# Performance work log

Hardware: AMD Instinct MI355X
Metric: run time of the kernel (lower is better)

The kernel has to match this reference:

```python
import jax, jax.numpy as jnp
import numpy as np
import math

B, C, H, W = 2, 512, 64, 64
NUM_HEADS = 8
D_K = C // NUM_HEADS
SCALE = 1.0 / math.sqrt(D_K)


def setup_inputs() -> dict:
    key = jax.random.key(0)
    ks = jax.random.split(key, 7)
    init = 0.02
    return {
        "x": jax.random.normal(ks[0], (B, C, H, W), dtype=jnp.float32),
        "Wq": jax.random.normal(ks[1], (C, C), dtype=jnp.float32) * init,
        "bq": jnp.zeros((C,), dtype=jnp.float32),
        "Wkv": jax.random.normal(ks[2], (2 * C, C), dtype=jnp.float32) * init,
        "bkv": jnp.zeros((2 * C,), dtype=jnp.float32),
        "Wp": jax.random.normal(ks[3], (C, C), dtype=jnp.float32) * init,
        "bp": jnp.zeros((C,), dtype=jnp.float32),
    }


def _conv1x1(x, w, b):
    # x: [b, c_in, h, w], w: [c_out, c_in] (1x1 conv kernel), b: [c_out]
    return jnp.einsum('bchw,oc->bohw', x, w) + b[None, :, None, None]


def reference(x, Wq, bq, Wkv, bkv, Wp, bp):
    b, c, h, w = x.shape
    l = h * w
    q = _conv1x1(x, Wq, bq)
    kv = _conv1x1(x, Wkv, bkv)
    k, v = jnp.split(kv, 2, axis=1)
    # reshape to [b, heads, d_k, l]
    q = q.reshape(b, NUM_HEADS, D_K, l)
    k = k.reshape(b, NUM_HEADS, D_K, l)
    v = v.reshape(b, NUM_HEADS, D_K, l)
    attn = jnp.einsum('bhct,bhcs->bhts', q, k) * SCALE  # [b,h,l,l]
    attn = jax.nn.softmax(attn, axis=-1)
    out = jnp.einsum('bhts,bhcs->bhct', attn, v)  # [b,h,d_k,l]
    out = out.reshape(b, c, h, w)
    out = _conv1x1(out, Wp, bp)
    return out
```

## Files before the change

kernel.cpp:

```cpp
#include <hip/hip_runtime.h>
#include <math.h>

#define L_SEQ 4096
#define C_DIM 512
#define NH 8
#define DK 64
#define NB 2
#define QSC 0.18033688011112042f

typedef _Float16 f16;
typedef _Float16 f16x8 __attribute__((ext_vector_type(8)));
typedef _Float16 f16x4 __attribute__((ext_vector_type(4)));
typedef __fp16 h16x2 __attribute__((ext_vector_type(2)));
typedef float f32x4 __attribute__((ext_vector_type(4)));
typedef float f32x16 __attribute__((ext_vector_type(16)));
typedef unsigned int u32;

__global__ __launch_bounds__(256) void prep(
    const float* __restrict__ X, const float* __restrict__ Wq,
    const float* __restrict__ Wkv, const float* __restrict__ Wp,
    f16* __restrict__ Xt, f16* __restrict__ Wqkh,
    f16* __restrict__ Wvh, f16* __restrict__ Wph)
{
    const int tid = threadIdx.x;
    const int z = blockIdx.z;
    if (z < 2) {
        __shared__ f16 Ts[64][72];
        const float* src = X + (size_t)z * C_DIM * L_SEQ;
        f16* dst = Xt + (size_t)z * L_SEQ * C_DIM;
        for (int tile = blockIdx.x; tile < 512; tile += gridDim.x) {
            const int c0 = (tile & 7) * 64;
            const int t0 = (tile >> 3) * 64;
            __syncthreads();
            #pragma unroll
            for (int p = 0; p < 4; ++p) {
                const int c = (tid >> 4) + p * 16;
                const int t = (tid & 15) * 4;
                const float4 v = *(const float4*)(src + (size_t)(c0 + c) * L_SEQ + t0 + t);
                Ts[t + 0][c] = (f16)v.x; Ts[t + 1][c] = (f16)v.y;
                Ts[t + 2][c] = (f16)v.z; Ts[t + 3][c] = (f16)v.w;
            }
            __syncthreads();
            #pragma unroll
            for (int p = 0; p < 2; ++p) {
                const int t = (tid >> 3) + p * 32;
                const int ch = (tid & 7) * 8;
                *(f16x8*)(dst + (size_t)(t0 + t) * C_DIM + c0 + ch) =
                    *(const f16x8*)&Ts[t][ch];
            }
        }
    } else {
        const float* srcs[4] = {Wq, Wkv, Wkv + 262144, Wp};
        f16* dsts[4] = {Wqkh, Wqkh + 262144, Wvh, Wph};
        #pragma unroll
        for (int s = 0; s < 4; ++s) {
            const float* sp = srcs[s]; f16* dp = dsts[s];
            for (int i = blockIdx.x * 256 + tid; i < 65536; i += gridDim.x * 256) {
                const float4 v = *(const float4*)(sp + (size_t)i * 4);
                f16x4 h; h[0] = (f16)v.x; h[1] = (f16)v.y; h[2] = (f16)v.z; h[3] = (f16)v.w;
                *(f16x4*)(dp + (size_t)i * 4) = h;
            }
        }
    }
}

__global__ __launch_bounds__(256) void qkv_mfma(
    const f16* __restrict__ Xt, const f16* __restrict__ Wqkv,
    const float* __restrict__ bq, const float* __restrict__ bkv,
    f16* __restrict__ Qh, f16* __restrict__ Kh, f16* __restrict__ Vh)
{
    __shared__ f16 As[128][40];
    __shared__ f16 Bs[128][40];
    const int tid = threadIdx.x;
    const int lane = tid & 63, w = tid >> 6;
    const int l15 = lane & 15, quad = lane >> 4;
    const int wy = w >> 1, wx = w & 1;
    const int mb0 = blockIdx.x * 128;
    const int n0  = blockIdx.y * 128;

    f32x4 acc[4][4] = {};
    const int row = tid >> 2, c8 = (tid & 3) * 8;
    const f16* aptr = Xt + (size_t)mb0 * 512;
    const f16* bptr = Wqkv + (size_t)n0 * 512;

    uint4 ga0 = *(const uint4*)(aptr + (size_t)row * 512 + c8);
    uint4 ga1 = *(const uint4*)(aptr + (size_t)(row + 64) * 512 + c8);
    uint4 gb0 = *(const uint4*)(bptr + (size_t)row * 512 + c8);
    uint4 gb1 = *(const uint4*)(bptr + (size_t)(row + 64) * 512 + c8);

    for (int k0 = 0; k0 < 512; k0 += 32) {
        __syncthreads();
        *(uint4*)&As[row][c8] = ga0;
        *(uint4*)&As[row + 64][c8] = ga1;
        *(uint4*)&Bs[row][c8] = gb0;
        *(uint4*)&Bs[row + 64][c8] = gb1;
        if (k0 + 32 < 512) {
            ga0 = *(const uint4*)(aptr + (size_t)row * 512 + k0 + 32 + c8);
            ga1 = *(const uint4*)(aptr + (size_t)(row + 64) * 512 + k0 + 32 + c8);
            gb0 = *(const uint4*)(bptr + (size_t)row * 512 + k0 + 32 + c8);
            gb1 = *(const uint4*)(bptr + (size_t)(row + 64) * 512 + k0 + 32 + c8);
        }
        __syncthreads();
        f16x8 af[4], bf[4];
        #pragma unroll
        for (int i = 0; i < 4; ++i)
            af[i] = *(const f16x8*)&As[wy * 64 + i * 16 + l15][quad * 8];
        #pragma unroll
        for (int n = 0; n < 4; ++n)
            bf[n] = *(const f16x8*)&Bs[wx * 64 + n * 16 + l15][quad * 8];
        #pragma unroll
        for (int i = 0; i < 4; ++i)
            #pragma unroll
            for (int n = 0; n < 4; ++n)
                acc[i][n] = __builtin_amdgcn_mfma_f32_16x16x32_f16(af[i], bf[n], acc[i][n], 0, 0, 0);
    }

    const int qp = ((quad & 1) << 1) | (quad >> 1);

    #pragma unroll
    for (int nn = 0; nn < 4; ++nn) {
        const int o = n0 + wx * 64 + nn * 16 + l15;
        if (o < 1024) {
            const bool isQ = (o < 512);
            const float bias = isQ ? bq[o] : bkv[o - 512];
            const int h = (o & 511) >> 6, d = o & 63;
            f16* base = isQ ? Qh : Kh;
            #pragma unroll
            for (int i = 0; i < 4; ++i) {
                const int tr = mb0 + wy * 64 + i * 16 + quad * 4;
                #pragma unroll
                for (int r = 0; r < 4; ++r) {
                    const int tg = tr + r;
                    const int bh = (tg >> 12) * NH + h;
                    float v = acc[i][nn][r] + bias;
                    if (isQ) v *= QSC;
                    base[((size_t)bh * L_SEQ + (tg & 4095)) * DK + d] = (f16)v;
                }
            }
        } else {
            const int c = o - 1024;
            const float bias = bkv[512 + c];
            const int h = c >> 6, d = c & 63;
            #pragma unroll
            for (int i = 0; i < 4; ++i) {
                const int trp = mb0 + wy * 64 + i * 16 + qp * 4;
                #pragma unroll
                for (int r = 0; r < 4; ++r) {
                    const int tq = trp + r;
                    const int bh = (tq >> 12) * NH + h;
                    const float v = acc[i][nn][r] + bias;
                    Vh[((size_t)bh * DK + d) * L_SEQ + (tq & 4095)] = (f16)v;
                }
            }
        }
    }
}

__global__ __launch_bounds__(256) void oproj2(
    const f16* __restrict__ Bsrc, const f16* __restrict__ Wh,
    const float* __restrict__ bias, float* __restrict__ outP)
{
    __shared__ f16 As[64][40];
    __shared__ f16 Bs[128][40];
    const int tid = threadIdx.x;
    const int lane = tid & 63, w = tid >> 6;
    const int l15 = lane & 15, quad = lane >> 4;
    const int wy = w >> 1, wx = w & 1;
    const int n0  = blockIdx.x * 128;
    const int mb0 = blockIdx.y * 64;

    f32x4 acc[2][4] = {};
    const int row = tid >> 2, c8 = (tid & 3) * 8;
    const f16* aptr = Wh + (size_t)mb0 * 512;
    const f16* bptr = Bsrc + (size_t)n0 * 512;

    uint4 ga0 = *(const uint4*)(aptr + (size_t)row * 512 + c8);
    uint4 gb0 = *(const uint4*)(bptr + (size_t)row * 512 + c8);
    uint4 gb1 = *(const uint4*)(bptr + (size_t)(row + 64) * 512 + c8);

    for (int k0 = 0; k0 < 512; k0 += 32) {
        __syncthreads();
        *(uint4*)&As[row][c8] = ga0;
        *(uint4*)&Bs[row][c8] = gb0;
        *(uint4*)&Bs[row + 64][c8] = gb1;
        if (k0 + 32 < 512) {
            ga0 = *(const uint4*)(aptr + (size_t)row * 512 + k0 + 32 + c8);
            gb0 = *(const uint4*)(bptr + (size_t)row * 512 + k0 + 32 + c8);
            gb1 = *(const uint4*)(bptr + (size_t)(row + 64) * 512 + k0 + 32 + c8);
        }
        __syncthreads();
        f16x8 af[2], bf[4];
        #pragma unroll
        for (int i = 0; i < 2; ++i)
            af[i] = *(const f16x8*)&As[wy * 32 + i * 16 + l15][quad * 8];
        #pragma unroll
        for (int n = 0; n < 4; ++n)
            bf[n] = *(const f16x8*)&Bs[wx * 64 + n * 16 + l15][quad * 8];
        #pragma unroll
        for (int i = 0; i < 2; ++i)
            #pragma unroll
            for (int n = 0; n < 4; ++n)
                acc[i][n] = __builtin_amdgcn_mfma_f32_16x16x32_f16(af[i], bf[n], acc[i][n], 0, 0, 0);
    }

    #pragma unroll
    for (int i = 0; i < 2; ++i) {
        #pragma unroll
        for (int r = 0; r < 4; ++r) {
            const int o = mb0 + wy * 32 + i * 16 + quad * 4 + r;
            const float bv = bias[o];
            #pragma unroll
            for (int nn = 0; nn < 4; ++nn) {
                const int tg = n0 + wx * 64 + nn * 16 + l15;
                outP[((size_t)(tg >> 12) * C_DIM + o) * L_SEQ + (tg & 4095)] =
                    acc[i][nn][r] + bv;
            }
        }
    }
}

__device__ __forceinline__ void gload_lds16(const char* g, char* l) {
    __builtin_amdgcn_global_load_lds(
        (const __attribute__((address_space(1))) void*)g,
        (__attribute__((address_space(3))) void*)l, 16, 0, 0);
}

union FR { u32 u[4]; f16x8 v; };

__device__ __forceinline__ void smax8(const f32x16& S, FR* fr, int base,
                                      float& rsv, h16x2 one2) {
    #pragma unroll
    for (int q = 0; q < 4; ++q) {
        const h16x2 a01 = __builtin_amdgcn_cvt_pkrtz(
            __builtin_amdgcn_exp2f(S[4 * q + 0]),
            __builtin_amdgcn_exp2f(S[4 * q + 1]));
        const h16x2 a23 = __builtin_amdgcn_cvt_pkrtz(
            __builtin_amdgcn_exp2f(S[4 * q + 2]),
            __builtin_amdgcn_exp2f(S[4 * q + 3]));
        rsv = __builtin_amdgcn_fdot2(a01, one2, rsv, false);
        rsv = __builtin_amdgcn_fdot2(a23, one2, rsv, false);
        union { h16x2 h; u32 u; } p0, p1; p0.h = a01; p1.h = a23;
        fr[base + (q >> 1)].u[(q & 1) * 2 + 0] = p0.u;
        fr[base + (q >> 1)].u[(q & 1) * 2 + 1] = p1.u;
    }
}

__global__ __launch_bounds__(256, 2) void flash16(
    const f16* __restrict__ Qh, const f16* __restrict__ Kh,
    const f16* __restrict__ Vh, f16* __restrict__ Opart,
    float* __restrict__ Lpart)
{
    __shared__ f16 KS[2][4096];
    __shared__ f16 VS[3][4096];
    const int tid = threadIdx.x;
    const int lane = tid & 63, w = tid >> 6;
    const int l31 = lane & 31, hl = lane >> 5;
    const int bh = blockIdx.x;
    const int t0 = blockIdx.y * 256;
    const int half = blockIdx.z;
    const int s_beg = half * 2048;
    const int wtb = t0 + w * 64;
    const f16* Qg = Qh + (size_t)bh * L_SEQ * DK;
    const char* Kg = (const char*)(Kh + (size_t)bh * L_SEQ * DK);
    const char* Vg = (const char*)(Vh + (size_t)bh * DK * L_SEQ);

    f16x8 qf0[4], qf1[4];
    #pragma unroll
    for (int kst = 0; kst < 4; ++kst) {
        qf0[kst] = *(const f16x8*)(Qg + (size_t)(wtb + l31) * DK + kst * 16 + hl * 8);
        qf1[kst] = *(const f16x8*)(Qg + (size_t)(wtb + 32 + l31) * DK + kst * 16 + hl * 8);
    }

    const int c0 = tid, c1 = tid + 256;
    const int kofs0 = (c0 >> 3) * 128  + (((c0 & 7) * 16) ^ (((c0 >> 3) & 7) << 4));
    const int kofs1 = (c1 >> 3) * 128  + (((c1 & 7) * 16) ^ (((c1 >> 3) & 7) << 4));
    const int vofs0 = (c0 >> 3) * 8192 + (((c0 & 7) * 16) ^ (((c0 >> 3) & 7) << 4));
    const int vofs1 = (c1 >> 3) * 8192 + (((c1 & 7) * 16) ^ (((c1 >> 3) & 7) << 4));
    const int lb0 = (w * 64) * 16, lb1 = (256 + w * 64) * 16;

    #define STAGE_K(kb, s0v) do {                                    \
        const char* kg_ = Kg + (size_t)(s0v) * 128;                  \
        char* kl_ = (char*)&KS[kb][0];                               \
        gload_lds16(kg_ + kofs0, kl_ + lb0);                         \
        gload_lds16(kg_ + kofs1, kl_ + lb1);                         \
    } while (0)
    #define STAGE_V(vOfs, s0v) do {                                  \
        const char* vg_ = Vg + (size_t)(s0v) * 2;                    \
        char* vl_ = (char*)&VS[0][0] + (vOfs);                       \
        gload_lds16(vg_ + vofs0, vl_ + lb0);                         \
        gload_lds16(vg_ + vofs1, vl_ + lb1);                         \
    } while (0)

    f32x16 O00 = {}, O01 = {}, O10 = {}, O11 = {};
    float rs0 = 0.f, rs1 = 0.f;
    h16x2 one2; one2[0] = (__fp16)1.f; one2[1] = (__fp16)1.f;
    FR frA0[4], frA1[4], frB0[4], frB1[4];

    STAGE_K(0, s_beg); STAGE_V(0, s_beg);
    __syncthreads();

    const int swz = (l31 & 7) << 4;
    const int rowA = l31 * 128, rowB = (32 + l31) * 128;

    #define QKBODY(s0v, kbR, kbS, DOSTG, DOPV, stO, pvO, frC0, frC1, frP0, frP1) do { \
        if (DOSTG) { STAGE_K(kbS, (s0v) + 64); STAGE_V(stO, (s0v) + 64); }  \
        const char* Kb = (const char*)&KS[kbR][0];                          \
        f16x8 kf[4];                                                        \
        _Pragma("unroll")                                                   \
        for (int kst = 0; kst < 4; ++kst)                                   \
            kf[kst] = *(const f16x8*)(Kb + rowA + ((kst * 32 + hl * 16) ^ swz)); \
        {                                                                   \
            f32x16 Sa0 = {}, Sa1 = {};                                      \
            __builtin_amdgcn_s_setprio(1);                                  \
            _Pragma("unroll")                                               \
            for (int kst = 0; kst < 4; ++kst) {                             \
                Sa0 = __builtin_amdgcn_mfma_f32_32x32x16_f16(kf[kst], qf0[kst], Sa0, 0, 0, 0); \
                Sa1 = __builtin_amdgcn_mfma_f32_32x32x16_f16(kf[kst], qf1[kst], Sa1, 0, 0, 0); \
            }                                                               \
            __builtin_amdgcn_s_setprio(0);                                  \
            _Pragma("unroll")                                               \
            for (int kst = 0; kst < 4; ++kst)                               \
                kf[kst] = *(const f16x8*)(Kb + rowB + ((kst * 32 + hl * 16) ^ swz)); \
            smax8(Sa0, frC0, 0, rs0, one2);                                 \
            smax8(Sa1, frC1, 0, rs1, one2);                                 \
        }                                                                   \
        __builtin_amdgcn_sched_barrier(0);                                  \
        {                                                                   \
            f32x16 Sb0 = {}, Sb1 = {};                                      \
            __builtin_amdgcn_s_setprio(1);                                  \
            _Pragma("unroll")                                               \
            for (int kst = 0; kst < 4; ++kst) {                             \
                Sb0 = __builtin_amdgcn_mfma_f32_32x32x16_f16(kf[kst], qf0[kst], Sb0, 0, 0, 0); \
                Sb1 = __builtin_amdgcn_mfma_f32_32x32x16_f16(kf[kst], qf1[kst], Sb1, 0, 0, 0); \
            }                                                               \
            if (DOPV) {                                                     \
                const char* Vb = (const char*)&VS[0][0] + (pvO);            \
                _Pragma("unroll")                                           \
                for (int kst = 0; kst < 4; ++kst) {                         \
                    const int ca = (kst * 32 + hl * 16) ^ swz;              \
                    const f16x8 v0 = *(const f16x8*)(Vb + rowA + ca);       \
                    const f16x8 v1 = *(const f16x8*)(Vb + rowB + ca);       \
                    O00 = __builtin_amdgcn_mfma_f32_32x32x16_f16(v0, frP0[kst].v, O00, 0, 0, 0); \
                    O01 = __builtin_amdgcn_mfma_f32_32x32x16_f16(v0, frP1[kst].v, O01, 0, 0, 0); \
                    O10 = __builtin_amdgcn_mfma_f32_32x32x16_f16(v1, frP0[kst].v, O10, 0, 0, 0); \
                    O11 = __builtin_amdgcn_mfma_f32_32x32x16_f16(v1, frP1[kst].v, O11, 0, 0, 0); \
                }                                                           \
            }                                                               \
            __builtin_amdgcn_s_setprio(0);                                  \
            smax8(Sb0, frC0, 2, rs0, one2);                                 \
            smax8(Sb1, frC1, 2, rs1, one2);                                 \
        }                                                                   \
        __syncthreads();                                                    \
    } while (0)

    QKBODY(s_beg, 0, 1, true, false, 8192, 0, frA0, frA1, frB0, frB1);

    int s0 = s_beg + 64;
    int stO = 16384, pvO = 0;
    #pragma unroll 1
    for (int p = 0; p < 15; ++p) {
        QKBODY(s0, 1, 0, true, true, stO, pvO, frB0, frB1, frA0, frA1);
        s0 += 64; stO = (stO == 16384) ? 0 : stO + 8192; pvO = (pvO == 16384) ? 0 : pvO + 8192;
        QKBODY(s0, 0, 1, true, true, stO, pvO, frA0, frA1, frB0, frB1);
        s0 += 64; stO = (stO == 16384) ? 0 : stO + 8192; pvO = (pvO == 16384) ? 0 : pvO + 8192;
    }
    QKBODY(s0, 1, 0, false, true, 0, pvO, frB0, frB1, frA0, frA1);

    {
        const char* Vb = (const char*)&VS[0][0] + 8192;
        __builtin_amdgcn_s_setprio(1);
        #pragma unroll
        for (int kst = 0; kst < 4; ++kst) {
            const int ca = (kst * 32 + hl * 16) ^ swz;
            const f16x8 v0 = *(const f16x8*)(Vb + rowA + ca);
            const f16x8 v1 = *(const f16x8*)(Vb + rowB + ca);
            O00 = __builtin_amdgcn_mfma_f32_32x32x16_f16(v0, frB0[kst].v, O00, 0, 0, 0);
            O01 = __builtin_amdgcn_mfma_f32_32x32x16_f16(v0, frB1[kst].v, O01, 0, 0, 0);
            O10 = __builtin_amdgcn_mfma_f32_32x32x16_f16(v1, frB0[kst].v, O10, 0, 0, 0);
            O11 = __builtin_amdgcn_mfma_f32_32x32x16_f16(v1, frB1[kst].v, O11, 0, 0, 0);
        }
        __builtin_amdgcn_s_setprio(0);
    }
    #undef QKBODY
    #undef STAGE_K
    #undef STAGE_V

    rs0 += __shfl_xor(rs0, 32, 64);
    rs1 += __shfl_xor(rs1, 32, 64);
    if (lane < 32) {
        float* Lp = Lpart + (size_t)(half * 16 + bh) * L_SEQ + wtb;
        Lp[l31] = rs0;
        Lp[32 + l31] = rs1;
    }

    f16* Op = Opart + (size_t)(half * 16 + bh) * DK * L_SEQ;
    #pragma unroll
    for (int r = 0; r < 16; ++r) {
        const int d = (r & 3) + 8 * (r >> 2) + 4 * hl;
        Op[(size_t)d * L_SEQ + wtb + l31] = (f16)O00[r];
        Op[(size_t)d * L_SEQ + wtb + 32 + l31] = (f16)O01[r];
        Op[(size_t)(32 + d) * L_SEQ + wtb + l31] = (f16)O10[r];
        Op[(size_t)(32 + d) * L_SEQ + wtb + 32 + l31] = (f16)O11[r];
    }
}

__global__ __launch_bounds__(256) void combine(
    const f16* __restrict__ Opart, const float* __restrict__ Lpart,
    f16* __restrict__ Oh)
{
    __shared__ f16 Ts[64][72];
    __shared__ float Linv[64];
    const int tid = threadIdx.x;
    const int bh = blockIdx.y, b = bh >> 3, h = bh & 7;
    const int t0 = blockIdx.x * 64;
    if (tid < 64) {
        const float lo = Lpart[(size_t)bh * L_SEQ + t0 + tid];
        const float hi = Lpart[(size_t)(16 + bh) * L_SEQ + t0 + tid];
        Linv[tid] = 1.f / (lo + hi);
    }
    __syncthreads();
    const f16* Plo = Opart + (size_t)bh * DK * L_SEQ;
    const f16* Phi = Opart + (size_t)(16 + bh) * DK * L_SEQ;
    const int d = tid >> 4;
    const int tt = (tid & 15) * 4;
    #pragma unroll
    for (int p = 0; p < 4; ++p) {
        const int dd = d + p * 16;
        const size_t off = (size_t)dd * L_SEQ + t0 + tt;
        const f16x4 lo = *(const f16x4*)(Plo + off);
        const f16x4 hi = *(const f16x4*)(Phi + off);
        #pragma unroll
        for (int j = 0; j < 4; ++j)
            Ts[tt + j][dd] = (f16)(((float)lo[j] + (float)hi[j]) * Linv[tt + j]);
    }
    __syncthreads();
    const int tr = tid >> 2, ch = (tid & 3) * 16;
    f16* dst = Oh + ((size_t)(b * L_SEQ + t0 + tr)) * C_DIM + h * DK + ch;
    *(f16x8*)dst = *(const f16x8*)&Ts[tr][ch];
    *(f16x8*)(dst + 8) = *(const f16x8*)&Ts[tr][ch + 8];
}

extern "C" void kernel_launch(void* const* d_in, const int* in_sizes, int n_in,
                              void* d_out, int out_size, void* d_ws, size_t ws_size,
                              hipStream_t stream) {
    (void)in_sizes; (void)n_in; (void)out_size; (void)ws_size;
    const float* x   = (const float*)d_in[0];
    const float* Wq  = (const float*)d_in[1];
    const float* bq  = (const float*)d_in[2];
    const float* Wkv = (const float*)d_in[3];
    const float* bkv = (const float*)d_in[4];
    const float* Wp  = (const float*)d_in[5];
    const float* bp  = (const float*)d_in[6];
    float* out = (float*)d_out;

    f16* Xt    = (f16*)d_ws;
    f16* Wqkh  = Xt + 4194304;
    f16* Wvh   = Wqkh + 524288;
    f16* Wph   = Wvh + 262144;
    f16* Qh    = Wph + 262144;
    f16* Kh    = Qh + 4194304;
    f16* Vh    = Kh + 4194304;
    f16* Oh    = Vh + 4194304;
    f16* Opart = Oh + 4194304;
    float* Lpart = (float*)(Opart + 8388608);

    prep<<<dim3(128, 1, 3), 256, 0, stream>>>(x, Wq, Wkv, Wp, Xt, Wqkh, Wvh, Wph);
    qkv_mfma<<<dim3(64, 12), 256, 0, stream>>>(Xt, Wqkh, bq, bkv, Qh, Kh, Vh);
    flash16<<<dim3(16, 16, 2), 256, 0, stream>>>(Qh, Kh, Vh, Opart, Lpart);
    combine<<<dim3(64, 16), 256, 0, stream>>>(Opart, Lpart, Oh);
    oproj2<<<dim3(64, 8), 256, 0, stream>>>(Oh, Wph, bp, out);
}
```

Baseline: 194.4 us.

## Drop split-KV in flash attention, halve per-wave query tile, fuse normalization

The flash kernel no longer splits the key range into two halves with a separate combine kernel. Each block now covers 128 queries (32 per wave) over the full key range and writes the normalized output directly in token-major layout. This removes the partial-output round trip through global memory and one kernel launch, while keeping the grid at 512 blocks. In exchange, each K/V tile loaded into LDS is reused across half as many queries, so the ratio of LDS traffic to MFMA work roughly doubles. Each block also runs a key loop twice as long.

```diff
diff --git a/kernel.cpp b/kernel.cpp
--- a/kernel.cpp
+++ b/kernel.cpp
@@ -247,8 +247,7 @@
 
 __global__ __launch_bounds__(256, 2) void flash16(
     const f16* __restrict__ Qh, const f16* __restrict__ Kh,
-    const f16* __restrict__ Vh, f16* __restrict__ Opart,
-    float* __restrict__ Lpart)
+    const f16* __restrict__ Vh, f16* __restrict__ Oh)
 {
     __shared__ f16 KS[2][4096];
     __shared__ f16 VS[3][4096];
@@ -256,20 +255,16 @@
     const int lane = tid & 63, w = tid >> 6;
     const int l31 = lane & 31, hl = lane >> 5;
     const int bh = blockIdx.x;
-    const int t0 = blockIdx.y * 256;
-    const int half = blockIdx.z;
-    const int s_beg = half * 2048;
-    const int wtb = t0 + w * 64;
+    const int t0 = blockIdx.y * 128;
+    const int wtb = t0 + w * 32;
     const f16* Qg = Qh + (size_t)bh * L_SEQ * DK;
     const char* Kg = (const char*)(Kh + (size_t)bh * L_SEQ * DK);
     const char* Vg = (const char*)(Vh + (size_t)bh * DK * L_SEQ);
 
-    f16x8 qf0[4], qf1[4];
+    f16x8 qf[4];
     #pragma unroll
-    for (int kst = 0; kst < 4; ++kst) {
-        qf0[kst] = *(const f16x8*)(Qg + (size_t)(wtb + l31) * DK + kst * 16 + hl * 8);
-        qf1[kst] = *(const f16x8*)(Qg + (size_t)(wtb + 32 + l31) * DK + kst * 16 + hl * 8);
-    }
+    for (int kst = 0; kst < 4; ++kst)
+        qf[kst] = *(const f16x8*)(Qg + (size_t)(wtb + l31) * DK + kst * 16 + hl * 8);
 
     const int c0 = tid, c1 = tid + 256;
     const int kofs0 = (c0 >> 3) * 128  + (((c0 & 7) * 16) ^ (((c0 >> 3) & 7) << 4));
@@ -291,18 +286,18 @@
         gload_lds16(vg_ + vofs1, vl_ + lb1);                         \
     } while (0)
 
-    f32x16 O00 = {}, O01 = {}, O10 = {}, O11 = {};
-    float rs0 = 0.f, rs1 = 0.f;
+    f32x16 O0 = {}, O1 = {};
+    float rs = 0.f;
     h16x2 one2; one2[0] = (__fp16)1.f; one2[1] = (__fp16)1.f;
-    FR frA0[4], frA1[4], frB0[4], frB1[4];
-
-    STAGE_K(0, s_beg); STAGE_V(0, s_beg);
+    FR frA[4], frB[4];
+
+    STAGE_K(0, 0); STAGE_V(0, 0);
     __syncthreads();
 
     const int swz = (l31 & 7) << 4;
     const int rowA = l31 * 128, rowB = (32 + l31) * 128;
 
-    #define QKBODY(s0v, kbR, kbS, DOSTG, DOPV, stO, pvO, frC0, frC1, frP0, frP1) do { \
+    #define QKBODY(s0v, kbR, kbS, DOSTG, DOPV, stO, pvO, frC, frP) do {     \
         if (DOSTG) { STAGE_K(kbS, (s0v) + 64); STAGE_V(stO, (s0v) + 64); }  \
         const char* Kb = (const char*)&KS[kbR][0];                          \
         f16x8 kf[4];                                                        \
@@ -310,29 +305,24 @@
         for (int kst = 0; kst < 4; ++kst)                                   \
             kf[kst] = *(const f16x8*)(Kb + rowA + ((kst * 32 + hl * 16) ^ swz)); \
         {                                                                   \
-            f32x16 Sa0 = {}, Sa1 = {};                                      \
+            f32x16 Sa = {};                                                 \
             __builtin_amdgcn_s_setprio(1);                                  \
             _Pragma("unroll")                                               \
-            for (int kst = 0; kst < 4; ++kst) {                             \
-                Sa0 = __builtin_amdgcn_mfma_f32_32x32x16_f16(kf[kst], qf0[kst], Sa0, 0, 0, 0); \
-                Sa1 = __builtin_amdgcn_mfma_f32_32x32x16_f16(kf[kst], qf1[kst], Sa1, 0, 0, 0); \
-            }                                                               \
+            for (int kst = 0; kst < 4; ++kst)                               \
+                Sa = __builtin_amdgcn_mfma_f32_32x32x16_f16(kf[kst], qf[kst], Sa, 0, 0, 0); \
             __builtin_amdgcn_s_setprio(0);                                  \
             _Pragma("unroll")                                               \
             for (int kst = 0; kst < 4; ++kst)                               \
                 kf[kst] = *(const f16x8*)(Kb + rowB + ((kst * 32 + hl * 16) ^ swz)); \
-            smax8(Sa0, frC0, 0, rs0, one2);                                 \
-            smax8(Sa1, frC1, 0, rs1, one2);                                 \
+            smax8(Sa, frC, 0, rs, one2);                                    \
         }                                                                   \
         __builtin_amdgcn_sched_barrier(0);                                  \
         {                                                                   \
-            f32x16 Sb0 = {}, Sb1 = {};                                      \
+            f32x16 Sb = {};                                                 \
             __builtin_amdgcn_s_setprio(1);                                  \
             _Pragma("unroll")                                               \
-            for (int kst = 0; kst < 4; ++kst) {                             \
-                Sb0 = __builtin_amdgcn_mfma_f32_32x32x16_f16(kf[kst], qf0[kst], Sb0, 0, 0, 0); \
-                Sb1 = __builtin_amdgcn_mfma_f32_32x32x16_f16(kf[kst], qf1[kst], Sb1, 0, 0, 0); \
-            }                                                               \
+            for (int kst = 0; kst < 4; ++kst)                               \
+                Sb = __builtin_amdgcn_mfma_f32_32x32x16_f16(kf[kst], qf[kst], Sb, 0, 0, 0); \
             if (DOPV) {                                                     \
                 const char* Vb = (const char*)&VS[0][0] + (pvO);            \
                 _Pragma("unroll")                                           \
@@ -340,44 +330,39 @@
                     const int ca = (kst * 32 + hl * 16) ^ swz;              \
                     const f16x8 v0 = *(const f16x8*)(Vb + rowA + ca);       \
                     const f16x8 v1 = *(const f16x8*)(Vb + rowB + ca);       \
-                    O00 = __builtin_amdgcn_mfma_f32_32x32x16_f16(v0, frP0[kst].v, O00, 0, 0, 0); \
-                    O01 = __builtin_amdgcn_mfma_f32_32x32x16_f16(v0, frP1[kst].v, O01, 0, 0, 0); \
-                    O10 = __builtin_amdgcn_mfma_f32_32x32x16_f16(v1, frP0[kst].v, O10, 0, 0, 0); \
-                    O11 = __builtin_amdgcn_mfma_f32_32x32x16_f16(v1, frP1[kst].v, O11, 0, 0, 0); \
+                    O0 = __builtin_amdgcn_mfma_f32_32x32x16_f16(v0, frP[kst].v, O0, 0, 0, 0); \
+                    O1 = __builtin_amdgcn_mfma_f32_32x32x16_f16(v1, frP[kst].v, O1, 0, 0, 0); \
                 }                                                           \
             }                                                               \
             __builtin_amdgcn_s_setprio(0);                                  \
-            smax8(Sb0, frC0, 2, rs0, one2);                                 \
-            smax8(Sb1, frC1, 2, rs1, one2);                                 \
+            smax8(Sb, frC, 2, rs, one2);                                    \
         }                                                                   \
         __syncthreads();                                                    \
     } while (0)
 
-    QKBODY(s_beg, 0, 1, true, false, 8192, 0, frA0, frA1, frB0, frB1);
-
-    int s0 = s_beg + 64;
+    QKBODY(0, 0, 1, true, false, 8192, 0, frA, frB);
+
+    int s0 = 64;
     int stO = 16384, pvO = 0;
     #pragma unroll 1
-    for (int p = 0; p < 15; ++p) {
-        QKBODY(s0, 1, 0, true, true, stO, pvO, frB0, frB1, frA0, frA1);
+    for (int p = 0; p < 31; ++p) {
+        QKBODY(s0, 1, 0, true, true, stO, pvO, frB, frA);
         s0 += 64; stO = (stO == 16384) ? 0 : stO + 8192; pvO = (pvO == 16384) ? 0 : pvO + 8192;
-        QKBODY(s0, 0, 1, true, true, stO, pvO, frA0, frA1, frB0, frB1);
+        QKBODY(s0, 0, 1, true, true, stO, pvO, frA, frB);
         s0 += 64; stO = (stO == 16384) ? 0 : stO + 8192; pvO = (pvO == 16384) ? 0 : pvO + 8192;
     }
-    QKBODY(s0, 1, 0, false, true, 0, pvO, frB0, frB1, frA0, frA1);
+    QKBODY(s0, 1, 0, false, true, 0, pvO, frB, frA);
 
     {
-        const char* Vb = (const char*)&VS[0][0] + 8192;
+        const char* Vb = (const char*)&VS[0][0];
         __builtin_amdgcn_s_setprio(1);
         #pragma unroll
         for (int kst = 0; kst < 4; ++kst) {
             const int ca = (kst * 32 + hl * 16) ^ swz;
             const f16x8 v0 = *(const f16x8*)(Vb + rowA + ca);
             const f16x8 v1 = *(const f16x8*)(Vb + rowB + ca);
-            O00 = __builtin_amdgcn_mfma_f32_32x32x16_f16(v0, frB0[kst].v, O00, 0, 0, 0);
-            O01 = __builtin_amdgcn_mfma_f32_32x32x16_f16(v0, frB1[kst].v, O01, 0, 0, 0);
-            O10 = __builtin_amdgcn_mfma_f32_32x32x16_f16(v1, frB0[kst].v, O10, 0, 0, 0);
-            O11 = __builtin_amdgcn_mfma_f32_32x32x16_f16(v1, frB1[kst].v, O11, 0, 0, 0);
+            O0 = __builtin_amdgcn_mfma_f32_32x32x16_f16(v0, frB[kst].v, O0, 0, 0, 0);
+            O1 = __builtin_amdgcn_mfma_f32_32x32x16_f16(v1, frB[kst].v, O1, 0, 0, 0);
         }
         __builtin_amdgcn_s_setprio(0);
     }
@@ -385,59 +370,22 @@
     #undef STAGE_K
     #undef STAGE_V
 
-    rs0 += __shfl_xor(rs0, 32, 64);
-    rs1 += __shfl_xor(rs1, 32, 64);
-    if (lane < 32) {
-        float* Lp = Lpart + (size_t)(half * 16 + bh) * L_SEQ + wtb;
-        Lp[l31] = rs0;
-        Lp[32 + l31] = rs1;
-    }
-
-    f16* Op = Opart + (size_t)(half * 16 + bh) * DK * L_SEQ;
+    rs += __shfl_xor(rs, 32, 64);
+    const float rinv = 1.f / rs;
+
+    const int b = bh >> 3, h = bh & 7;
+    f16* OhP = Oh + ((size_t)(b * L_SEQ + wtb + l31)) * C_DIM + h * DK;
     #pragma unroll
-    for (int r = 0; r < 16; ++r) {
-        const int d = (r & 3) + 8 * (r >> 2) + 4 * hl;
-        Op[(size_t)d * L_SEQ + wtb + l31] = (f16)O00[r];
-        Op[(size_t)d * L_SEQ + wtb + 32 + l31] = (f16)O01[r];
-        Op[(size_t)(32 + d) * L_SEQ + wtb + l31] = (f16)O10[r];
-        Op[(size_t)(32 + d) * L_SEQ + wtb + 32 + l31] = (f16)O11[r];
-    }
-}
-
-__global__ __launch_bounds__(256) void combine(
-    const f16* __restrict__ Opart, const float* __restrict__ Lpart,
-    f16* __restrict__ Oh)
-{
-    __shared__ f16 Ts[64][72];
-    __shared__ float Linv[64];
-    const int tid = threadIdx.x;
-    const int bh = blockIdx.y, b = bh >> 3, h = bh & 7;
-    const int t0 = blockIdx.x * 64;
-    if (tid < 64) {
-        const float lo = Lpart[(size_t)bh * L_SEQ + t0 + tid];
-        const float hi = Lpart[(size_t)(16 + bh) * L_SEQ + t0 + tid];
-        Linv[tid] = 1.f / (lo + hi);
-    }
-    __syncthreads();
-    const f16* Plo = Opart + (size_t)bh * DK * L_SEQ;
-    const f16* Phi = Opart + (size_t)(16 + bh) * DK * L_SEQ;
-    const int d = tid >> 4;
-    const int tt = (tid & 15) * 4;
-    #pragma unroll
-    for (int p = 0; p < 4; ++p) {
-        const int dd = d + p * 16;
-        const size_t off = (size_t)dd * L_SEQ + t0 + tt;
-        const f16x4 lo = *(const f16x4*)(Plo + off);
-        const f16x4 hi = *(const f16x4*)(Phi + off);
-        #pragma unroll
-        for (int j = 0; j < 4; ++j)
-            Ts[tt + j][dd] = (f16)(((float)lo[j] + (float)hi[j]) * Linv[tt + j]);
-    }
-    __syncthreads();
-    const int tr = tid >> 2, ch = (tid & 3) * 16;
-    f16* dst = Oh + ((size_t)(b * L_SEQ + t0 + tr)) * C_DIM + h * DK + ch;
-    *(f16x8*)dst = *(const f16x8*)&Ts[tr][ch];
-    *(f16x8*)(dst + 8) = *(const f16x8*)&Ts[tr][ch + 8];
+    for (int run = 0; run < 4; ++run) {
+        f16x4 v0, v1;
+        #pragma unroll
+        for (int j = 0; j < 4; ++j) {
+            v0[j] = (f16)(O0[run * 4 + j] * rinv);
+            v1[j] = (f16)(O1[run * 4 + j] * rinv);
+        }
+        *(f16x4*)(OhP + run * 8 + 4 * hl) = v0;
+        *(f16x4*)(OhP + 32 + run * 8 + 4 * hl) = v1;
+    }
 }
 
 extern "C" void kernel_launch(void* const* d_in, const int* in_sizes, int n_in,
@@ -461,12 +409,9 @@
     f16* Kh    = Qh + 4194304;
     f16* Vh    = Kh + 4194304;
     f16* Oh    = Vh + 4194304;
-    f16* Opart = Oh + 4194304;
-    float* Lpart = (float*)(Opart + 8388608);
 
     prep<<<dim3(128, 1, 3), 256, 0, stream>>>(x, Wq, Wkv, Wp, Xt, Wqkh, Wvh, Wph);
     qkv_mfma<<<dim3(64, 12), 256, 0, stream>>>(Xt, Wqkh, bq, bkv, Qh, Kh, Vh);
-    flash16<<<dim3(16, 16, 2), 256, 0, stream>>>(Qh, Kh, Vh, Opart, Lpart);
-    combine<<<dim3(64, 16), 256, 0, stream>>>(Opart, Lpart, Oh);
+    flash16<<<dim3(16, 32), 256, 0, stream>>>(Qh, Kh, Vh, Oh);
     oproj2<<<dim3(64, 8), 256, 0, stream>>>(Oh, Wph, bp, out);
 }
```

Result: no change. 194.0 us (-0.2%).
